# Optimization experiments

Hardware: AMD Instinct MI355X
Metric: run time of the kernel (lower is better)

Reference implementation:

```python
import jax, jax.numpy as jnp
import numpy as np

H = 16          # heads_num
D = 1024        # model_dim
HD = D // H     # per-head dim
NEG = -1e9


def setup_inputs() -> dict:
    key = jax.random.key(0)
    ks = jax.random.split(key, 12)
    B, S = 4, 1024
    inp = {
        "q": jax.random.normal(ks[0], (B, S, D), jnp.float32),
        "k": jax.random.normal(ks[1], (B, S, D), jnp.float32),
        "v": jax.random.normal(ks[2], (B, S, D), jnp.float32),
        "mask": jnp.ones((B, 1, S), jnp.int32),
    }
    s = 1.0 / np.sqrt(D)
    inp["Wq"] = jax.random.normal(ks[3], (D, D), jnp.float32) * s
    inp["bq"] = jnp.zeros((D,), jnp.float32)
    inp["Wk"] = jax.random.normal(ks[4], (D, D), jnp.float32) * s
    inp["bk"] = jnp.zeros((D,), jnp.float32)
    inp["Wv"] = jax.random.normal(ks[5], (D, D), jnp.float32) * s
    inp["bv"] = jnp.zeros((D,), jnp.float32)
    inp["Wo"] = jax.random.normal(ks[6], (D, D), jnp.float32) * s
    inp["bo"] = jnp.zeros((D,), jnp.float32)
    return inp


def _split_heads(x, B):
    # [B, S, D] -> [B, H, S, HD]
    return x.reshape(B, -1, H, HD).transpose(0, 2, 1, 3)


def reference(q, k, v, mask, Wq, bq, Wk, bk, Wv, bv, Wo, bo):
    B = q.shape[0]
    qh = _split_heads(q @ Wq.T + bq, B)  # [B,H,Sq,HD]
    kh = _split_heads(k @ Wk.T + bk, B)  # [B,H,Sk,HD]
    vh = _split_heads(v @ Wv.T + bv, B)  # [B,H,Sk,HD]
    scores = jnp.einsum("bhqd,bhkd->bhqk", qh, kh) / np.sqrt(HD)
    # mask [B,1,Sk] -> unsqueeze head dim -> [B,1,1,Sk], broadcast over q and heads
    scores = jnp.where(mask[:, None] == 0, NEG, scores)
    attn = jax.nn.softmax(scores, axis=-1)  # dropout in eval mode = identity
    ctx = jnp.einsum("bhqk,bhkd->bhqd", attn, vh)
    out = ctx.transpose(0, 2, 1, 3).reshape(B, -1, D)
    return out @ Wo.T + bo
```

## Files before the change

### kernel.cpp

```cpp
#include <hip/hip_runtime.h>
#include <hip/hip_bf16.h>
#include <math.h>

typedef __bf16 bf16;
typedef __bf16 bf16x8 __attribute__((ext_vector_type(8)));
typedef __bf16 bf16x2 __attribute__((ext_vector_type(2)));
typedef float f32x4 __attribute__((ext_vector_type(4)));
typedef float f32x16 __attribute__((ext_vector_type(16)));

#define D_MODEL 1024
#define SEQ 1024
#define BATCH 4
#define NHEAD 16
#define MTOT (BATCH*SEQ)

#define QSCALE 0.18033688011112042f
#define MASKNEG -1e9f

__global__ void cast_all(const float* __restrict__ s0, const float* __restrict__ s1,
                         const float* __restrict__ s2, const float* __restrict__ s3,
                         const float* __restrict__ s4, const float* __restrict__ s5,
                         const float* __restrict__ s6,
                         bf16* d0, bf16* d1, bf16* d2, bf16* d3, bf16* d4, bf16* d5, bf16* d6) {
    int z = blockIdx.y;
    const float* s; bf16* d; int n;
    switch (z) {
        case 0: s = s0; d = d0; n = MTOT * D_MODEL; break;
        case 1: s = s1; d = d1; n = MTOT * D_MODEL; break;
        case 2: s = s2; d = d2; n = MTOT * D_MODEL; break;
        case 3: s = s3; d = d3; n = D_MODEL * D_MODEL; break;
        case 4: s = s4; d = d4; n = D_MODEL * D_MODEL; break;
        case 5: s = s5; d = d5; n = D_MODEL * D_MODEL; break;
        default: s = s6; d = d6; n = D_MODEL * D_MODEL; break;
    }
    int idx = (blockIdx.x * blockDim.x + threadIdx.x) * 8;
    int stride = gridDim.x * blockDim.x * 8;
    for (int i = idx; i < n; i += stride) {
        const float4* p = (const float4*)(s + i);
        float4 a = p[0], b = p[1];
        bf16x8 o;
        o[0] = (bf16)a.x; o[1] = (bf16)a.y; o[2] = (bf16)a.z; o[3] = (bf16)a.w;
        o[4] = (bf16)b.x; o[5] = (bf16)b.y; o[6] = (bf16)b.z; o[7] = (bf16)b.w;
        *(bf16x8*)(d + i) = o;
    }
}

template<typename OT, int MODE>
__global__ __launch_bounds__(256, 2)
void gemm_bt(const bf16* __restrict__ A0, const bf16* __restrict__ A1, const bf16* __restrict__ A2,
             const bf16* __restrict__ W0, const bf16* __restrict__ W1, const bf16* __restrict__ W2,
             const float* __restrict__ bias0, const float* __restrict__ bias1, const float* __restrict__ bias2,
             OT* __restrict__ O0, OT* __restrict__ O1, OT* __restrict__ O2) {
    constexpr int BK = 32;
    constexpr int K = D_MODEL, N = D_MODEL;
    __shared__ alignas(16) bf16 As[128 * BK];
    __shared__ alignas(16) bf16 Bs[128 * BK];

    int z = (MODE == 0) ? blockIdx.z : 0;
    const bf16* A = (z == 0) ? A0 : (z == 1) ? A1 : A2;
    const bf16* W = (z == 0) ? W0 : (z == 1) ? W1 : W2;
    const float* bias = (z == 0) ? bias0 : (z == 1) ? bias1 : bias2;
    OT* Out = (z == 0) ? O0 : (z == 1) ? O1 : O2;

    int tid = threadIdx.x;
    int lane = tid & 63, w = tid >> 6;
    int l15 = lane & 15, l4 = lane >> 4;
    int m0 = blockIdx.x * 128;
    int n0 = blockIdx.y * 128;
    int wm = w >> 1, wn = w & 1;

    f32x4 acc[4][4] = {};

    int srow = lane >> 2;
    int scol = (lane & 3) * 8;

    for (int k0 = 0; k0 < K; k0 += BK) {
        __syncthreads();
#pragma unroll
        for (int i = 0; i < 2; ++i) {
            int seg = w * 2 + i;
            int row = seg * 16 + srow;
            const bf16* srcA = A + (size_t)(m0 + row) * K + k0 + scol;
            const bf16* srcB = W + (size_t)(n0 + row) * K + k0 + scol;
            __builtin_amdgcn_global_load_lds(
                (const __attribute__((address_space(1))) void*)srcA,
                (__attribute__((address_space(3))) void*)(As + seg * 512), 16, 0, 0);
            __builtin_amdgcn_global_load_lds(
                (const __attribute__((address_space(1))) void*)srcB,
                (__attribute__((address_space(3))) void*)(Bs + seg * 512), 16, 0, 0);
        }
        __syncthreads();

        const bf16* pa = As + (wm * 64 + l15) * BK + l4 * 8;
        const bf16* pb = Bs + (wn * 64 + l15) * BK + l4 * 8;
        bf16x8 af[4], bv[4];
#pragma unroll
        for (int m = 0; m < 4; ++m) af[m] = *(const bf16x8*)(pa + m * 16 * BK);
#pragma unroll
        for (int n = 0; n < 4; ++n) bv[n] = *(const bf16x8*)(pb + n * 16 * BK);
#pragma unroll
        for (int m = 0; m < 4; ++m)
#pragma unroll
            for (int n = 0; n < 4; ++n)
                acc[m][n] = __builtin_amdgcn_mfma_f32_16x16x32_bf16(af[m], bv[n], acc[m][n], 0, 0, 0);
    }

    float bload[4];
#pragma unroll
    for (int n = 0; n < 4; ++n) bload[n] = bias[n0 + wn * 64 + n * 16 + l15];

    if (MODE == 0 && z == 2) {
#pragma unroll
        for (int m = 0; m < 4; ++m) {
            int row = m0 + wm * 64 + m * 16 + l4 * 4;
#pragma unroll
            for (int n = 0; n < 4; ++n) {
                int col = n0 + wn * 64 + n * 16 + l15;
                float bl = bload[n];
#pragma unroll
                for (int r = 0; r < 4; ++r) {
                    float vv = acc[m][n][r] + bl;
                    int rr = row + r;
                    int bb = rr >> 10, s = rr & 1023;
                    Out[((size_t)(bb * 1024 + col)) * 1024 + s] = (OT)vv;
                }
            }
        }
    } else {
        const float sc = (MODE == 0 && z == 0) ? QSCALE : 1.0f;
#pragma unroll
        for (int m = 0; m < 4; ++m) {
            int row = m0 + wm * 64 + m * 16 + l4 * 4;
#pragma unroll
            for (int n = 0; n < 4; ++n) {
                int col = n0 + wn * 64 + n * 16 + l15;
                float bl = bload[n];
#pragma unroll
                for (int r = 0; r < 4; ++r) {
                    float vv = (acc[m][n][r] + bl) * sc;
                    Out[(size_t)(row + r) * N + col] = (OT)vv;
                }
            }
        }
    }
}

__device__ __forceinline__ unsigned pkbf(float lo, float hi2) {
    bf16x2 t; t[0] = (bf16)lo; t[1] = (bf16)hi2;
    return __builtin_bit_cast(unsigned, t);
}

__global__ __launch_bounds__(256, 2)
void attn_fwd(const bf16* __restrict__ Qp, const bf16* __restrict__ Kp,
              const bf16* __restrict__ VT, const int* __restrict__ maskp,
              bf16* __restrict__ ctx) {
    __shared__ alignas(16) bf16 Kls[2][64 * 64];
    __shared__ alignas(16) bf16 Vls[2][64 * 64];
    __shared__ alignas(16) float madd[2][64];

    int tid = threadIdx.x;
    int lane = tid & 63, w = tid >> 6;
    int l31 = lane & 31, hi = lane >> 5;

    int fid = blockIdx.x;
    int by = (fid & 7) * 8 + ((fid >> 3) >> 3);
    int bx = (fid >> 3) & 7;
    int b = by >> 4, h = by & 15;
    int q0 = bx * 128;

    bf16x8 qf[4];
    {
        const bf16* qb = Qp + ((size_t)(b * SEQ + q0 + w * 32 + l31)) * D_MODEL + h * 64 + hi * 8;
#pragma unroll
        for (int ks = 0; ks < 4; ++ks) qf[ks] = *(const bf16x8*)(qb + ks * 16);
    }

    f32x16 oacc0 = {}, oacc1 = {};
    float lsum = 0.f;

    auto stage = [&](int buf, int kt) {
        int kv0 = kt * 64;
#pragma unroll
        for (int i = 0; i < 2; ++i) {
            int seg = w * 2 + i;
            int row = seg * 8 + (lane >> 3);
            int cs = ((lane & 7) ^ (row & 7)) * 8;
            const bf16* srcK = Kp + ((size_t)(b * SEQ + kv0 + row)) * D_MODEL + h * 64 + cs;
            __builtin_amdgcn_global_load_lds(
                (const __attribute__((address_space(1))) void*)srcK,
                (__attribute__((address_space(3))) void*)(&Kls[buf][seg * 512]), 16, 0, 0);
            const bf16* srcV = VT + ((size_t)(b * 1024 + h * 64 + row)) * SEQ + kv0 + cs;
            __builtin_amdgcn_global_load_lds(
                (const __attribute__((address_space(1))) void*)srcV,
                (__attribute__((address_space(3))) void*)(&Vls[buf][seg * 512]), 16, 0, 0);
        }
        if (tid < 64) {
            madd[buf][tid] = maskp[b * SEQ + kv0 + tid] ? 0.f : MASKNEG;
        }
    };

    stage(0, 0);
    __syncthreads();

    for (int kt = 0; kt < SEQ / 64; ++kt) {
        int cur = kt & 1;
        if (kt + 1 < SEQ / 64) stage(cur ^ 1, kt + 1);

        f32x16 p0 = {}, p1 = {};
        __builtin_amdgcn_s_setprio(1);
#pragma unroll
        for (int ks = 0; ks < 4; ++ks) {
            int slot = ((2 * ks + hi) ^ (l31 & 7)) * 8;
            bf16x8 k0 = *(const bf16x8*)(&Kls[cur][l31 * 64 + slot]);
            bf16x8 k1 = *(const bf16x8*)(&Kls[cur][(32 + l31) * 64 + slot]);
            p0 = __builtin_amdgcn_mfma_f32_32x32x16_bf16(k0, qf[ks], p0, 0, 0, 0);
            p1 = __builtin_amdgcn_mfma_f32_32x32x16_bf16(k1, qf[ks], p1, 0, 0, 0);
        }
        __builtin_amdgcn_s_setprio(0);

        const float* mb = &madd[cur][0];
        float acc_s = 0.f;
#pragma unroll
        for (int g = 0; g < 4; ++g) {
            f32x4 mk0 = *(const f32x4*)(mb + g * 8 + hi * 4);
            f32x4 mk1 = *(const f32x4*)(mb + 32 + g * 8 + hi * 4);
            float s0 = 0.f, s1 = 0.f;
#pragma unroll
            for (int c = 0; c < 4; ++c) {
                int r = g * 4 + c;
                float e0 = exp2f(p0[r] + mk0[c]);
                float e1 = exp2f(p1[r] + mk1[c]);
                p0[r] = e0; p1[r] = e1;
                s0 += e0; s1 += e1;
            }
            acc_s += s0 + s1;
        }
        acc_s += __shfl_xor(acc_s, 32);
        lsum += acc_s;

        union FragU { bf16x8 v; unsigned u[4]; };
        FragU pa0, pa1, pa2, pa3;
#define PKSW(PV, RA, RB, DST)  { \
            unsigned a_ = pkbf(PV[RA], PV[(RA) + 1]); \
            unsigned b_ = pkbf(PV[RB], PV[(RB) + 1]); \
            auto rr_ = __builtin_amdgcn_permlane32_swap(a_, b_, false, false); \
            DST.u[((RA) & 3) >> 1] = rr_[0]; DST.u[(((RA) & 3) >> 1) + 2] = rr_[1]; }
        PKSW(p0, 0, 4,  pa0);
        PKSW(p0, 2, 6,  pa0);
        PKSW(p0, 8, 12, pa1);
        PKSW(p0, 10, 14, pa1);
        PKSW(p1, 0, 4,  pa2);
        PKSW(p1, 2, 6,  pa2);
        PKSW(p1, 8, 12, pa3);
        PKSW(p1, 10, 14, pa3);
#undef PKSW

        __builtin_amdgcn_s_setprio(1);
#pragma unroll
        for (int ks = 0; ks < 4; ++ks) {
            bf16x8 pav = (ks == 0) ? pa0.v : (ks == 1) ? pa1.v : (ks == 2) ? pa2.v : pa3.v;
            int slot = ((2 * ks + hi) ^ (l31 & 7)) * 8;
            bf16x8 v0 = *(const bf16x8*)(&Vls[cur][l31 * 64 + slot]);
            bf16x8 v1 = *(const bf16x8*)(&Vls[cur][(32 + l31) * 64 + slot]);
            oacc0 = __builtin_amdgcn_mfma_f32_32x32x16_bf16(pav, v0, oacc0, 0, 0, 0);
            oacc1 = __builtin_amdgcn_mfma_f32_32x32x16_bf16(pav, v1, oacc1, 0, 0, 0);
        }
        __builtin_amdgcn_s_setprio(0);

        __syncthreads();
    }

#pragma unroll
    for (int g = 0; g < 4; ++g) {
#pragma unroll
        for (int c = 0; c < 4; ++c) {
            int r = g * 4 + c;
            int qloc = c + g * 8 + hi * 4;
            float sden = __shfl(lsum, qloc);
            float inv = 1.0f / sden;
            int qg = q0 + w * 32 + qloc;
            size_t base = ((size_t)(b * SEQ + qg)) * D_MODEL + h * 64;
            ctx[base + l31]      = (bf16)(oacc0[r] * inv);
            ctx[base + 32 + l31] = (bf16)(oacc1[r] * inv);
        }
    }
}

extern "C" void kernel_launch(void* const* d_in, const int* in_sizes, int n_in,
                              void* d_out, int out_size, void* d_ws, size_t ws_size,
                              hipStream_t stream) {
    const float* q  = (const float*)d_in[0];
    const float* k  = (const float*)d_in[1];
    const float* v  = (const float*)d_in[2];
    const int* mask = (const int*)d_in[3];
    const float* Wq = (const float*)d_in[4];
    const float* bq = (const float*)d_in[5];
    const float* Wk = (const float*)d_in[6];
    const float* bk = (const float*)d_in[7];
    const float* Wv = (const float*)d_in[8];
    const float* bv = (const float*)d_in[9];
    const float* Wo = (const float*)d_in[10];
    const float* bo = (const float*)d_in[11];
    float* out = (float*)d_out;

    char* ws = (char*)d_ws;
    size_t szQKV = (size_t)MTOT * D_MODEL * sizeof(bf16);
    size_t szW = (size_t)D_MODEL * D_MODEL * sizeof(bf16);
    bf16* qb  = (bf16*)ws; ws += szQKV;
    bf16* kb  = (bf16*)ws; ws += szQKV;
    bf16* vb  = (bf16*)ws; ws += szQKV;
    bf16* Wqb = (bf16*)ws; ws += szW;
    bf16* Wkb = (bf16*)ws; ws += szW;
    bf16* Wvb = (bf16*)ws; ws += szW;
    bf16* Wob = (bf16*)ws; ws += szW;
    bf16* Qp  = (bf16*)ws; ws += szQKV;
    bf16* Kp  = (bf16*)ws; ws += szQKV;
    bf16* VT  = (bf16*)ws; ws += szQKV;
    bf16* ctx = (bf16*)ws; ws += szQKV;

    dim3 gc(512, 7, 1);
    cast_all<<<gc, 256, 0, stream>>>(q, k, v, Wq, Wk, Wv, Wo,
                                     qb, kb, vb, Wqb, Wkb, Wvb, Wob);

    dim3 g1(MTOT / 128, D_MODEL / 128, 3);
    gemm_bt<bf16, 0><<<g1, 256, 0, stream>>>(qb, kb, vb, Wqb, Wkb, Wvb,
                                             bq, bk, bv, Qp, Kp, VT);

    attn_fwd<<<dim3(512), 256, 0, stream>>>(Qp, Kp, VT, mask, ctx);

    dim3 g3(MTOT / 128, D_MODEL / 128, 1);
    gemm_bt<float, 1><<<g3, 256, 0, stream>>>(ctx, ctx, ctx, Wob, Wob, Wob,
                                              bo, bo, bo, out, out, out);
}
```

Before: 111.5 us.

## Fuse activation cast into QKV GEMM, widen attention blocks, skip mask when unmasked

The separate fp32-to-bf16 cast of q/k/v is removed. The QKV GEMM now loads fp32 activations directly and converts them into LDS, which avoids writing and re-reading three bf16 activation copies. The attention kernel moves to 512 threads with 256 query rows per block and loads the whole mask row once. Per-tile ballot flags let it skip the mask add when a tile is fully unmasked. The GEMMs get launch bounds of 3 blocks per CU, at the cost of synchronous fp32 loads in the GEMM mainloop instead of async global-to-LDS copies for A.

```diff
diff --git a/kernel.cpp b/kernel.cpp
--- a/kernel.cpp
+++ b/kernel.cpp
@@ -17,22 +17,18 @@
 #define QSCALE 0.18033688011112042f
 #define MASKNEG -1e9f
 
-__global__ void cast_all(const float* __restrict__ s0, const float* __restrict__ s1,
-                         const float* __restrict__ s2, const float* __restrict__ s3,
-                         const float* __restrict__ s4, const float* __restrict__ s5,
-                         const float* __restrict__ s6,
-                         bf16* d0, bf16* d1, bf16* d2, bf16* d3, bf16* d4, bf16* d5, bf16* d6) {
+__global__ void cast_w(const float* __restrict__ s0, const float* __restrict__ s1,
+                       const float* __restrict__ s2, const float* __restrict__ s3,
+                       bf16* d0, bf16* d1, bf16* d2, bf16* d3) {
     int z = blockIdx.y;
-    const float* s; bf16* d; int n;
+    const float* s; bf16* d;
     switch (z) {
-        case 0: s = s0; d = d0; n = MTOT * D_MODEL; break;
-        case 1: s = s1; d = d1; n = MTOT * D_MODEL; break;
-        case 2: s = s2; d = d2; n = MTOT * D_MODEL; break;
-        case 3: s = s3; d = d3; n = D_MODEL * D_MODEL; break;
-        case 4: s = s4; d = d4; n = D_MODEL * D_MODEL; break;
-        case 5: s = s5; d = d5; n = D_MODEL * D_MODEL; break;
-        default: s = s6; d = d6; n = D_MODEL * D_MODEL; break;
-    }
+        case 0: s = s0; d = d0; break;
+        case 1: s = s1; d = d1; break;
+        case 2: s = s2; d = d2; break;
+        default: s = s3; d = d3; break;
+    }
+    const int n = D_MODEL * D_MODEL;
     int idx = (blockIdx.x * blockDim.x + threadIdx.x) * 8;
     int stride = gridDim.x * blockDim.x * 8;
     for (int i = idx; i < n; i += stride) {
@@ -45,22 +41,21 @@
     }
 }
 
-template<typename OT, int MODE>
-__global__ __launch_bounds__(256, 2)
-void gemm_bt(const bf16* __restrict__ A0, const bf16* __restrict__ A1, const bf16* __restrict__ A2,
-             const bf16* __restrict__ W0, const bf16* __restrict__ W1, const bf16* __restrict__ W2,
-             const float* __restrict__ bias0, const float* __restrict__ bias1, const float* __restrict__ bias2,
-             OT* __restrict__ O0, OT* __restrict__ O1, OT* __restrict__ O2) {
+__global__ __launch_bounds__(256, 3)
+void gemm_qkv(const float* __restrict__ A0, const float* __restrict__ A1, const float* __restrict__ A2,
+              const bf16* __restrict__ W0, const bf16* __restrict__ W1, const bf16* __restrict__ W2,
+              const float* __restrict__ bias0, const float* __restrict__ bias1, const float* __restrict__ bias2,
+              bf16* __restrict__ O0, bf16* __restrict__ O1, bf16* __restrict__ O2) {
     constexpr int BK = 32;
-    constexpr int K = D_MODEL, N = D_MODEL;
+    constexpr int K = D_MODEL;
     __shared__ alignas(16) bf16 As[128 * BK];
     __shared__ alignas(16) bf16 Bs[128 * BK];
 
-    int z = (MODE == 0) ? blockIdx.z : 0;
-    const bf16* A = (z == 0) ? A0 : (z == 1) ? A1 : A2;
+    int z = blockIdx.z;
+    const float* A = (z == 0) ? A0 : (z == 1) ? A1 : A2;
     const bf16* W = (z == 0) ? W0 : (z == 1) ? W1 : W2;
     const float* bias = (z == 0) ? bias0 : (z == 1) ? bias1 : bias2;
-    OT* Out = (z == 0) ? O0 : (z == 1) ? O1 : O2;
+    bf16* Out = (z == 0) ? O0 : (z == 1) ? O1 : O2;
 
     int tid = threadIdx.x;
     int lane = tid & 63, w = tid >> 6;
@@ -71,6 +66,99 @@
 
     f32x4 acc[4][4] = {};
 
+    int srow = lane >> 2;
+    int scol = (lane & 3) * 8;
+
+    for (int k0 = 0; k0 < K; k0 += BK) {
+        __syncthreads();
+#pragma unroll
+        for (int i = 0; i < 2; ++i) {
+            int seg = w * 2 + i;
+            int row = seg * 16 + srow;
+            const bf16* srcB = W + (size_t)(n0 + row) * K + k0 + scol;
+            __builtin_amdgcn_global_load_lds(
+                (const __attribute__((address_space(1))) void*)srcB,
+                (__attribute__((address_space(3))) void*)(Bs + seg * 512), 16, 0, 0);
+            const float* srcA = A + (size_t)(m0 + row) * K + k0 + scol;
+            float4 fa = *(const float4*)srcA;
+            float4 fb = *(const float4*)(srcA + 4);
+            bf16x8 o;
+            o[0] = (bf16)fa.x; o[1] = (bf16)fa.y; o[2] = (bf16)fa.z; o[3] = (bf16)fa.w;
+            o[4] = (bf16)fb.x; o[5] = (bf16)fb.y; o[6] = (bf16)fb.z; o[7] = (bf16)fb.w;
+            *(bf16x8*)(As + seg * 512 + lane * 8) = o;
+        }
+        __syncthreads();
+
+        const bf16* pa = As + (wm * 64 + l15) * BK + l4 * 8;
+        const bf16* pb = Bs + (wn * 64 + l15) * BK + l4 * 8;
+        bf16x8 af[4], bv[4];
+#pragma unroll
+        for (int m = 0; m < 4; ++m) af[m] = *(const bf16x8*)(pa + m * 16 * BK);
+#pragma unroll
+        for (int n = 0; n < 4; ++n) bv[n] = *(const bf16x8*)(pb + n * 16 * BK);
+#pragma unroll
+        for (int m = 0; m < 4; ++m)
+#pragma unroll
+            for (int n = 0; n < 4; ++n)
+                acc[m][n] = __builtin_amdgcn_mfma_f32_16x16x32_bf16(af[m], bv[n], acc[m][n], 0, 0, 0);
+    }
+
+    float bload[4];
+#pragma unroll
+    for (int n = 0; n < 4; ++n) bload[n] = bias[n0 + wn * 64 + n * 16 + l15];
+
+    if (z == 2) {
+#pragma unroll
+        for (int m = 0; m < 4; ++m) {
+            int row = m0 + wm * 64 + m * 16 + l4 * 4;
+#pragma unroll
+            for (int n = 0; n < 4; ++n) {
+                int col = n0 + wn * 64 + n * 16 + l15;
+                float bl = bload[n];
+#pragma unroll
+                for (int r = 0; r < 4; ++r) {
+                    float vv = acc[m][n][r] + bl;
+                    int rr = row + r;
+                    int bb = rr >> 10, s = rr & 1023;
+                    Out[((size_t)(bb * 1024 + col)) * 1024 + s] = (bf16)vv;
+                }
+            }
+        }
+    } else {
+        const float sc = (z == 0) ? QSCALE : 1.0f;
+#pragma unroll
+        for (int m = 0; m < 4; ++m) {
+            int row = m0 + wm * 64 + m * 16 + l4 * 4;
+#pragma unroll
+            for (int n = 0; n < 4; ++n) {
+                int col = n0 + wn * 64 + n * 16 + l15;
+                float bl = bload[n];
+#pragma unroll
+                for (int r = 0; r < 4; ++r) {
+                    float vv = (acc[m][n][r] + bl) * sc;
+                    Out[(size_t)(row + r) * D_MODEL + col] = (bf16)vv;
+                }
+            }
+        }
+    }
+}
+
+__global__ __launch_bounds__(256, 3)
+void gemm_out(const bf16* __restrict__ A, const bf16* __restrict__ W,
+              const float* __restrict__ bias, float* __restrict__ Out) {
+    constexpr int BK = 32;
+    constexpr int K = D_MODEL;
+    __shared__ alignas(16) bf16 As[128 * BK];
+    __shared__ alignas(16) bf16 Bs[128 * BK];
+
+    int tid = threadIdx.x;
+    int lane = tid & 63, w = tid >> 6;
+    int l15 = lane & 15, l4 = lane >> 4;
+    int m0 = blockIdx.x * 128;
+    int n0 = blockIdx.y * 128;
+    int wm = w >> 1, wn = w & 1;
+
+    f32x4 acc[4][4] = {};
     int srow = lane >> 2;
     int scol = (lane & 3) * 8;
 
@@ -108,39 +196,16 @@
     float bload[4];
 #pragma unroll
     for (int n = 0; n < 4; ++n) bload[n] = bias[n0 + wn * 64 + n * 16 + l15];
-
-    if (MODE == 0 && z == 2) {
-#pragma unroll
-        for (int m = 0; m < 4; ++m) {
-            int row = m0 + wm * 64 + m * 16 + l4 * 4;
-#pragma unroll
-            for (int n = 0; n < 4; ++n) {
-                int col = n0 + wn * 64 + n * 16 + l15;
-                float bl = bload[n];
-#pragma unroll
-                for (int r = 0; r < 4; ++r) {
-                    float vv = acc[m][n][r] + bl;
-                    int rr = row + r;
-                    int bb = rr >> 10, s = rr & 1023;
-                    Out[((size_t)(bb * 1024 + col)) * 1024 + s] = (OT)vv;
-                }
-            }
-        }
-    } else {
-        const float sc = (MODE == 0 && z == 0) ? QSCALE : 1.0f;
-#pragma unroll
-        for (int m = 0; m < 4; ++m) {
-            int row = m0 + wm * 64 + m * 16 + l4 * 4;
-#pragma unroll
-            for (int n = 0; n < 4; ++n) {
-                int col = n0 + wn * 64 + n * 16 + l15;
-                float bl = bload[n];
-#pragma unroll
-                for (int r = 0; r < 4; ++r) {
-                    float vv = (acc[m][n][r] + bl) * sc;
-                    Out[(size_t)(row + r) * N + col] = (OT)vv;
-                }
-            }
+#pragma unroll
+    for (int m = 0; m < 4; ++m) {
+        int row = m0 + wm * 64 + m * 16 + l4 * 4;
+#pragma unroll
+        for (int n = 0; n < 4; ++n) {
+            int col = n0 + wn * 64 + n * 16 + l15;
+            float bl = bload[n];
+#pragma unroll
+            for (int r = 0; r < 4; ++r)
+                Out[(size_t)(row + r) * D_MODEL + col] = acc[m][n][r] + bl;
         }
     }
 }
@@ -150,23 +215,38 @@
     return __builtin_bit_cast(unsigned, t);
 }
 
-__global__ __launch_bounds__(256, 2)
+__global__ __launch_bounds__(512, 2)
 void attn_fwd(const bf16* __restrict__ Qp, const bf16* __restrict__ Kp,
               const bf16* __restrict__ VT, const int* __restrict__ maskp,
               bf16* __restrict__ ctx) {
     __shared__ alignas(16) bf16 Kls[2][64 * 64];
     __shared__ alignas(16) bf16 Vls[2][64 * 64];
-    __shared__ alignas(16) float madd[2][64];
+    __shared__ alignas(16) float madd2[SEQ];
+    __shared__ int tflag[16];
 
     int tid = threadIdx.x;
     int lane = tid & 63, w = tid >> 6;
     int l31 = lane & 31, hi = lane >> 5;
 
     int fid = blockIdx.x;
-    int by = (fid & 7) * 8 + ((fid >> 3) >> 3);
-    int bx = (fid >> 3) & 7;
+    int xcd = fid & 7, idx = fid >> 3;
+    int by = xcd * 8 + (idx >> 2);
+    int bx = idx & 3;
     int b = by >> 4, h = by & 15;
-    int q0 = bx * 128;
+    int q0 = bx * 256;
+
+    {
+        int m0v = maskp[b * SEQ + tid];
+        int m1v = maskp[b * SEQ + 512 + tid];
+        madd2[tid] = m0v ? 0.f : MASKNEG;
+        madd2[512 + tid] = m1v ? 0.f : MASKNEG;
+        unsigned long long b0 = __ballot(m0v != 0);
+        unsigned long long b1 = __ballot(m1v != 0);
+        if (lane == 0) {
+            tflag[w] = (b0 == ~0ull);
+            tflag[8 + w] = (b1 == ~0ull);
+        }
+    }
 
     bf16x8 qf[4];
     {
@@ -180,23 +260,16 @@
 
     auto stage = [&](int buf, int kt) {
         int kv0 = kt * 64;
-#pragma unroll
-        for (int i = 0; i < 2; ++i) {
-            int seg = w * 2 + i;
-            int row = seg * 8 + (lane >> 3);
-            int cs = ((lane & 7) ^ (row & 7)) * 8;
-            const bf16* srcK = Kp + ((size_t)(b * SEQ + kv0 + row)) * D_MODEL + h * 64 + cs;
-            __builtin_amdgcn_global_load_lds(
-                (const __attribute__((address_space(1))) void*)srcK,
-                (__attribute__((address_space(3))) void*)(&Kls[buf][seg * 512]), 16, 0, 0);
-            const bf16* srcV = VT + ((size_t)(b * 1024 + h * 64 + row)) * SEQ + kv0 + cs;
-            __builtin_amdgcn_global_load_lds(
-                (const __attribute__((address_space(1))) void*)srcV,
-                (__attribute__((address_space(3))) void*)(&Vls[buf][seg * 512]), 16, 0, 0);
-        }
-        if (tid < 64) {
-            madd[buf][tid] = maskp[b * SEQ + kv0 + tid] ? 0.f : MASKNEG;
-        }
+        int row = w * 8 + (lane >> 3);
+        int cs = ((lane & 7) ^ (row & 7)) * 8;
+        const bf16* srcK = Kp + ((size_t)(b * SEQ + kv0 + row)) * D_MODEL + h * 64 + cs;
+        __builtin_amdgcn_global_load_lds(
+            (const __attribute__((address_space(1))) void*)srcK,
+            (__attribute__((address_space(3))) void*)(&Kls[buf][w * 512]), 16, 0, 0);
+        const bf16* srcV = VT + ((size_t)(b * 1024 + h * 64 + row)) * SEQ + kv0 + cs;
+        __builtin_amdgcn_global_load_lds(
+            (const __attribute__((address_space(1))) void*)srcV,
+            (__attribute__((address_space(3))) void*)(&Vls[buf][w * 512]), 16, 0, 0);
     };
 
     stage(0, 0);
@@ -218,23 +291,46 @@
         }
         __builtin_amdgcn_s_setprio(0);
 
-        const float* mb = &madd[cur][0];
-        float acc_s = 0.f;
-#pragma unroll
-        for (int g = 0; g < 4; ++g) {
-            f32x4 mk0 = *(const f32x4*)(mb + g * 8 + hi * 4);
-            f32x4 mk1 = *(const f32x4*)(mb + 32 + g * 8 + hi * 4);
-            float s0 = 0.f, s1 = 0.f;
-#pragma unroll
-            for (int c = 0; c < 4; ++c) {
-                int r = g * 4 + c;
-                float e0 = exp2f(p0[r] + mk0[c]);
-                float e1 = exp2f(p1[r] + mk1[c]);
-                p0[r] = e0; p1[r] = e1;
-                s0 += e0; s1 += e1;
+        float a0 = 0.f, a1 = 0.f, a2 = 0.f, a3 = 0.f;
+        if (tflag[kt]) {
+#pragma unroll
+            for (int g = 0; g < 4; ++g) {
+                float s0 = 0.f, s1 = 0.f;
+#pragma unroll
+                for (int c = 0; c < 4; ++c) {
+                    int r = g * 4 + c;
+                    float e0 = exp2f(p0[r]);
+                    float e1 = exp2f(p1[r]);
+                    p0[r] = e0; p1[r] = e1;
+                    s0 += e0; s1 += e1;
+                }
+                if (g == 0) a0 = s0 + s1;
+                else if (g == 1) a1 = s0 + s1;
+                else if (g == 2) a2 = s0 + s1;
+                else a3 = s0 + s1;
             }
-            acc_s += s0 + s1;
-        }
+        } else {
+            const float* mb = &madd2[kt * 64];
+#pragma unroll
+            for (int g = 0; g < 4; ++g) {
+                f32x4 mk0 = *(const f32x4*)(mb + g * 8 + hi * 4);
+                f32x4 mk1 = *(const f32x4*)(mb + 32 + g * 8 + hi * 4);
+                float s0 = 0.f, s1 = 0.f;
+#pragma unroll
+                for (int c = 0; c < 4; ++c) {
+                    int r = g * 4 + c;
+                    float e0 = exp2f(p0[r] + mk0[c]);
+                    float e1 = exp2f(p1[r] + mk1[c]);
+                    p0[r] = e0; p1[r] = e1;
+                    s0 += e0; s1 += e1;
+                }
+                if (g == 0) a0 = s0 + s1;
+                else if (g == 1) a1 = s0 + s1;
+                else if (g == 2) a2 = s0 + s1;
+                else a3 = s0 + s1;
+            }
+        }
+        float acc_s = (a0 + a1) + (a2 + a3);
         acc_s += __shfl_xor(acc_s, 32);
         lsum += acc_s;
 
@@ -306,9 +402,6 @@
     char* ws = (char*)d_ws;
     size_t szQKV = (size_t)MTOT * D_MODEL * sizeof(bf16);
     size_t szW = (size_t)D_MODEL * D_MODEL * sizeof(bf16);
-    bf16* qb  = (bf16*)ws; ws += szQKV;
-    bf16* kb  = (bf16*)ws; ws += szQKV;
-    bf16* vb  = (bf16*)ws; ws += szQKV;
     bf16* Wqb = (bf16*)ws; ws += szW;
     bf16* Wkb = (bf16*)ws; ws += szW;
     bf16* Wvb = (bf16*)ws; ws += szW;
@@ -318,17 +411,15 @@
     bf16* VT  = (bf16*)ws; ws += szQKV;
     bf16* ctx = (bf16*)ws; ws += szQKV;
 
-    dim3 gc(512, 7, 1);
-    cast_all<<<gc, 256, 0, stream>>>(q, k, v, Wq, Wk, Wv, Wo,
-                                     qb, kb, vb, Wqb, Wkb, Wvb, Wob);
+    dim3 gc(256, 4, 1);
+    cast_w<<<gc, 256, 0, stream>>>(Wq, Wk, Wv, Wo, Wqb, Wkb, Wvb, Wob);
 
     dim3 g1(MTOT / 128, D_MODEL / 128, 3);
-    gemm_bt<bf16, 0><<<g1, 256, 0, stream>>>(qb, kb, vb, Wqb, Wkb, Wvb,
-                                             bq, bk, bv, Qp, Kp, VT);
-
-    attn_fwd<<<dim3(512), 256, 0, stream>>>(Qp, Kp, VT, mask, ctx);
+    gemm_qkv<<<g1, 256, 0, stream>>>(q, k, v, Wqb, Wkb, Wvb,
+                                     bq, bk, bv, Qp, Kp, VT);
+
+    attn_fwd<<<dim3(256), 512, 0, stream>>>(Qp, Kp, VT, mask, ctx);
 
     dim3 g3(MTOT / 128, D_MODEL / 128, 1);
-    gemm_bt<float, 1><<<g3, 256, 0, stream>>>(ctx, ctx, ctx, Wob, Wob, Wob,
-                                              bo, bo, bo, out, out, out);
-}
+    gemm_out<<<g3, 256, 0, stream>>>(ctx, Wob, bo, out);
+}
```

Result: no change. 111.1 us (-0.4%).
